# Optimization experiments

Measured on AMD Instinct MI355X. Metric: run time of the kernel, lower is better.

The kernel has to match this reference:

```python
import jax, jax.numpy as jnp
import numpy as np

K = 4        # maximum_fertility + 1
OOV_ID = 1
HIDDEN = 512


def setup_inputs() -> dict:
    key = jax.random.key(0)
    ks = jax.random.split(key, 8)
    B, S, D, E, H, V = 4, 128, 512, 256, HIDDEN, 32000
    return {
        "embedded_input": jax.random.normal(ks[0], (B, S, D), jnp.float32),
        "input_mask": jnp.ones((B, S), jnp.int32),
        "emb_table": jax.random.normal(ks[1], (V, E), jnp.float32) * 0.02,
        "W_ih": jax.random.normal(ks[2], (4 * H, D + E), jnp.float32) * 0.02,
        "b_ih": jax.random.normal(ks[3], (4 * H,), jnp.float32) * 0.02,
        "W_hh": jax.random.normal(ks[4], (4 * H, H), jnp.float32) * 0.02,
        "b_hh": jax.random.normal(ks[5], (4 * H,), jnp.float32) * 0.02,
        "W_out": jax.random.normal(ks[6], (V, H), jnp.float32) * 0.02,
        "b_out": jax.random.normal(ks[7], (V,), jnp.float32) * 0.02,
    }


def reference(embedded_input, input_mask, emb_table, W_ih, b_ih, W_hh, b_hh, W_out, b_out):
    B, S, D = embedded_input.shape
    V, E = emb_table.shape
    H = HIDDEN
    N = B * S
    x = embedded_input.reshape(N, D)                      # (N, D)
    h0 = jnp.zeros((N, H), embedded_input.dtype)
    c0 = jnp.zeros((N, H), embedded_input.dtype)
    # initial last_output: one-hot at OOV id (prob mass 1.0 on oov)
    last0 = jnp.zeros((N, V), embedded_input.dtype).at[:, OOV_ID].set(1.0)

    def step(carry, _):
        h, c, last = carry
        # embedding_bag soft mix over full vocab == weighted sum == matmul
        emb_last = last @ emb_table                        # (N, E)
        inp = jnp.concatenate([x, emb_last], axis=1)       # (N, D+E)
        gates = inp @ W_ih.T + b_ih + h @ W_hh.T + b_hh    # (N, 4H)
        i, f, g, o = jnp.split(gates, 4, axis=1)           # torch LSTMCell gate order
        i = jax.nn.sigmoid(i)
        f = jax.nn.sigmoid(f)
        g = jnp.tanh(g)
        o = jax.nn.sigmoid(o)
        c_new = f * c + i * g
        h_new = o * jnp.tanh(c_new)
        # dropout=0 / eval -> dropout mask is all ones (no-op)
        logits = h_new @ W_out.T + b_out                   # (N, V)
        logp = jax.nn.log_softmax(logits, axis=-1)
        return (h_new, c_new, jnp.exp(logp)), logp

    _, outs = jax.lax.scan(step, (h0, c0, last0), None, length=K)  # (K, N, V)
    return outs.transpose(1, 0, 2).reshape(B, S, K, V)
```

## Files before the change

### kernel.cpp

```cpp
#include <hip/hip_runtime.h>
#include <hip/hip_bf16.h>
#include <math.h>

#define N_ROWS 512
#define D_IN   512
#define E_EMB  256
#define H_DIM  512
#define G_DIM  2048
#define V_DIM  32000
#define IN_LD  1280
#define K_STEPS 4
#define OOV_ID 1
#define TBK 64
#define EMB_SPLIT 50
#define EMB_CHUNK 640
#define SEGSTRIDE 512

typedef __attribute__((ext_vector_type(4))) float f32x4;
typedef __attribute__((ext_vector_type(8))) short bf16x8;
typedef __attribute__((ext_vector_type(8))) _Float16 f16x8;

__device__ inline short f2b(float v) {
    __hip_bfloat16 h = __float2bfloat16(v);
    return *reinterpret_cast<short*>(&h);
}

__device__ inline void gload_lds(const short* g, short* l) {
    __builtin_amdgcn_global_load_lds(
        (const __attribute__((address_space(1))) void*)g,
        (__attribute__((address_space(3))) void*)l, 16, 0, 0);
}

template<int TBM, int TBN, int WR_, int WC_, int MODE>
__global__ __launch_bounds__(WR_ * WC_ * 64) void k_gemm(
    const short* __restrict__ A, int lda,
    const short* __restrict__ B, int ldb,
    const float* __restrict__ bias,
    float* __restrict__ C, size_t ldc, int Kc,
    float2* __restrict__ stats,
    float* __restrict__ cstate, short* __restrict__ hdst)
{
    constexpr int NW = WR_ * WC_;
    constexpr int WMT = TBM / WR_, WNT = TBN / WC_;
    constexpr int WM = WMT / 16, WN = WNT / 16;
    __shared__ short As[TBM * 64];
    __shared__ short Bs[TBN * 64];
    const int tid = threadIdx.x;
    const int lane = tid & 63, wid = tid >> 6;
    const int wr = wid % WR_, wc = wid / WR_;
    const int quad = lane >> 4, l16 = lane & 15;
    const int m0 = blockIdx.y * TBM, n0 = blockIdx.x * TBN;
    const int kbase = blockIdx.z * Kc;
    const int lrow = lane >> 3;
    const int lsw  = ((lane & 7) ^ lrow) * 8;

    f32x4 acc[WM][WN];
#pragma unroll
    for (int i = 0; i < WM; ++i)
#pragma unroll
        for (int j = 0; j < WN; ++j)
#pragma unroll
            for (int r = 0; r < 4; ++r) acc[i][j][r] = 0.0f;

    for (int kt = 0; kt < Kc; kt += TBK) {
        const int k0 = kbase + kt;
#pragma unroll
        for (int ch = wid; ch < TBM / 8; ch += NW)
            gload_lds(&A[(size_t)(m0 + ch * 8 + lrow) * lda + k0 + lsw], &As[ch * 512]);
#pragma unroll
        for (int ch = wid; ch < TBN / 8; ch += NW)
            gload_lds(&B[(size_t)(n0 + ch * 8 + lrow) * ldb + k0 + lsw], &Bs[ch * 512]);
        __syncthreads();
#pragma unroll
        for (int ks = 0; ks < 2; ++ks) {
            bf16x8 af[WM], bfv[WN];
#pragma unroll
            for (int i = 0; i < WM; ++i) {
                int rr = wr * WMT + i * 16 + l16;
                af[i] = *(const bf16x8*)&As[rr * 64 + (((ks * 4 + quad) ^ (l16 & 7)) * 8)];
            }
#pragma unroll
            for (int j = 0; j < WN; ++j) {
                int rr = wc * WNT + j * 16 + l16;
                bfv[j] = *(const bf16x8*)&Bs[rr * 64 + (((ks * 4 + quad) ^ (l16 & 7)) * 8)];
            }
#pragma unroll
            for (int i = 0; i < WM; ++i)
#pragma unroll
                for (int j = 0; j < WN; ++j)
                    acc[i][j] = __builtin_amdgcn_mfma_f32_16x16x32_bf16(af[i], bfv[j], acc[i][j], 0, 0, 0);
        }
        __syncthreads();
    }

    if constexpr (MODE == 3) {
        float* Cp = C + (size_t)blockIdx.z * N_ROWS * ldc;
#pragma unroll
        for (int i = 0; i < WM; ++i)
#pragma unroll
            for (int j = 0; j < WN; ++j) {
                const int n = n0 + wc * WNT + j * 16 + l16;
#pragma unroll
                for (int r = 0; r < 4; ++r) {
                    const int m = m0 + wr * WMT + i * 16 + quad * 4 + r;
                    Cp[(size_t)m * ldc + n] = acc[i][j][r];
                }
            }
    } else if constexpr (MODE == 2) {
        float bv[WN];
#pragma unroll
        for (int j = 0; j < WN; ++j) bv[j] = bias[n0 + j * 16 + l16];
        const int jj = (n0 >> 2) + l16;
#pragma unroll
        for (int i = 0; i < WM; ++i) {
#pragma unroll
            for (int r = 0; r < 4; ++r) {
                const int m = m0 + wr * WMT + i * 16 + quad * 4 + r;
                float gi = acc[i][0][r] + bv[0];
                float gf = acc[i][1][r] + bv[1];
                float gg = acc[i][2][r] + bv[2];
                float go = acc[i][3][r] + bv[3];
                float i_ = 1.0f / (1.0f + expf(-gi));
                float f_ = 1.0f / (1.0f + expf(-gf));
                float g_ = tanhf(gg);
                float o_ = 1.0f / (1.0f + expf(-go));
                const size_t ci = (size_t)m * H_DIM + jj;
                float cn = f_ * cstate[ci] + i_ * g_;
                cstate[ci] = cn;
                hdst[(size_t)m * IN_LD + (D_IN + E_EMB) + jj] = f2b(o_ * tanhf(cn));
            }
        }
    } else if constexpr (MODE == 4) {
        _Float16* Ch = (_Float16*)C;
        float bv[WN];
#pragma unroll
        for (int j = 0; j < WN; ++j) bv[j] = bias[n0 + wc * WNT + j * 16 + l16];
#pragma unroll
        for (int i = 0; i < WM; ++i) {
            float rm[4] = {-1e30f, -1e30f, -1e30f, -1e30f};
            float rs[4] = {0.f, 0.f, 0.f, 0.f};
#pragma unroll
            for (int j = 0; j < WN; ++j)
#pragma unroll
                for (int r = 0; r < 4; ++r)
                    rm[r] = fmaxf(rm[r], acc[i][j][r] + bv[j]);
#pragma unroll
            for (int j = 0; j < WN; ++j) {
                const int n = n0 + wc * WNT + j * 16 + l16;
#pragma unroll
                for (int r = 0; r < 4; ++r) {
                    const int m = m0 + wr * WMT + i * 16 + quad * 4 + r;
                    float z = acc[i][j][r] + bv[j];
                    rs[r] += __expf(z - rm[r]);
                    Ch[(size_t)m * ldc + n] = (_Float16)z;
                }
            }
#pragma unroll
            for (int mask = 1; mask < 16; mask <<= 1) {
#pragma unroll
                for (int r = 0; r < 4; ++r) {
                    float om = __shfl_xor(rm[r], mask);
                    float os = __shfl_xor(rs[r], mask);
                    float nm = fmaxf(rm[r], om);
                    rs[r] = rs[r] * __expf(rm[r] - nm) + os * __expf(om - nm);
                    rm[r] = nm;
                }
            }
            if (l16 == 0) {
                const int seg = (n0 + wc * WNT) >> 6;
#pragma unroll
                for (int r = 0; r < 4; ++r) {
                    const int m = m0 + wr * WMT + i * 16 + quad * 4 + r;
                    stats[(size_t)m * SEGSTRIDE + seg] = make_float2(rm[r], rs[r]);
                }
            }
        }
    } else {
        float bv[WN];
#pragma unroll
        for (int j = 0; j < WN; ++j) bv[j] = bias[n0 + wc * WNT + j * 16 + l16];
#pragma unroll
        for (int i = 0; i < WM; ++i)
#pragma unroll
            for (int j = 0; j < WN; ++j) {
                const int n = n0 + wc * WNT + j * 16 + l16;
#pragma unroll
                for (int r = 0; r < 4; ++r) {
                    const int m = m0 + wr * WMT + i * 16 + quad * 4 + r;
                    C[(size_t)m * ldc + n] = acc[i][j][r] + bv[j];
                }
            }
    }
}

__global__ __launch_bounds__(256) void k_prep(
    const float* __restrict__ x, const float* __restrict__ emb_table,
    const float* __restrict__ W_ih, const float* __restrict__ W_hh,
    const float* __restrict__ b_ih, const float* __restrict__ b_hh,
    const float* __restrict__ W_out,
    short* __restrict__ Abuf, short* __restrict__ Wg, float* __restrict__ bsum,
    short* __restrict__ Wout16, float* __restrict__ c)
{
    const int idx0 = blockIdx.x * 256 + threadIdx.x;
    const int gs = gridDim.x * 256;
    const float4* W4 = (const float4*)W_out;
    for (int i = idx0; i < V_DIM * H_DIM / 4; i += gs) {
        float4 v = W4[i];
        short4 o;
        o.x = f2b(v.x); o.y = f2b(v.y); o.z = f2b(v.z); o.w = f2b(v.w);
        ((short4*)Wout16)[i] = o;
    }
    for (int i = idx0; i < G_DIM * IN_LD; i += gs) {
        int rp = i / IN_LD, k = i - rp * IN_LD;
        int j = ((rp >> 6) << 4) | (rp & 15);
        int gate = (rp >> 4) & 3;
        int g = gate * H_DIM + j;
        float v = (k < D_IN + E_EMB) ? W_ih[(size_t)g * (D_IN + E_EMB) + k]
                                     : W_hh[(size_t)g * H_DIM + (k - (D_IN + E_EMB))];
        Wg[i] = f2b(v);
    }
    for (int i = idx0; i < G_DIM; i += gs) {
        int j = ((i >> 6) << 4) | (i & 15);
        int gate = (i >> 4) & 3;
        int g = gate * H_DIM + j;
        bsum[i] = b_ih[g] + b_hh[g];
    }
    for (int i = idx0; i < N_ROWS * IN_LD; i += gs) {
        int n = i / IN_LD, col = i - n * IN_LD;
        float v;
        if (col < D_IN)              v = x[(size_t)n * D_IN + col];
        else if (col < D_IN + E_EMB) v = emb_table[(size_t)OOV_ID * E_EMB + (col - D_IN)];
        else                         v = 0.0f;
        Abuf[i] = f2b(v);
    }
    for (int i = idx0; i < N_ROWS * H_DIM; i += gs) c[i] = 0.0f;
}

__global__ __launch_bounds__(256) void k_trans(const float* __restrict__ emb,
                                               short* __restrict__ embT)
{
    __shared__ float tile[64][65];
    const int v0 = blockIdx.x * 64, e0 = blockIdx.y * 64;
    const int tid = threadIdx.x;
#pragma unroll
    for (int i = 0; i < 16; ++i) {
        int idx = tid + i * 256;
        int vr = idx >> 6, ec = idx & 63;
        tile[vr][ec] = emb[(size_t)(v0 + vr) * E_EMB + e0 + ec];
    }
    __syncthreads();
#pragma unroll
    for (int i = 0; i < 16; ++i) {
        int idx = tid + i * 256;
        int er = idx >> 6, vc = idx & 63;
        embT[(size_t)(e0 + er) * V_DIM + v0 + vc] = f2b(tile[vc][er]);
    }
}

__global__ __launch_bounds__(256) void k_embred(const float* __restrict__ ep,
                                                short* __restrict__ Abuf)
{
    int idx = blockIdx.x * 256 + threadIdx.x;
    int n = idx >> 8, e = idx & 255;
    float s0 = 0.f, s1 = 0.f;
#pragma unroll
    for (int z = 0; z < EMB_SPLIT; z += 2) {
        s0 += ep[((size_t)z * N_ROWS + n) * E_EMB + e];
        s1 += ep[((size_t)(z + 1) * N_ROWS + n) * E_EMB + e];
    }
    Abuf[(size_t)n * IN_LD + D_IN + e] = f2b(s0 + s1);
}

__global__ __launch_bounds__(256) void k_lse(const float2* __restrict__ stats,
                                             float* __restrict__ lse)
{
    const int tid = threadIdx.x;
    const int lane = tid & 63, wid = tid >> 6;
    const int n = blockIdx.x * 4 + wid;

    float m = -1e30f, s = 0.0f;
    for (int sg = lane; sg < V_DIM / 64; sg += 64) {
        float2 p = stats[(size_t)n * SEGSTRIDE + sg];
        float nm = fmaxf(m, p.x);
        s = s * __expf(m - nm) + p.y * __expf(p.x - nm);
        m = nm;
    }
#pragma unroll
    for (int mask = 32; mask > 0; mask >>= 1) {
        float om = __shfl_xor(m, mask);
        float os = __shfl_xor(s, mask);
        float nm = fmaxf(m, om);
        s = s * __expf(m - nm) + os * __expf(om - nm);
        m = nm;
    }
    if (lane == 0) lse[n] = m + __logf(s);
}

__global__ __launch_bounds__(256) void k_finish(const _Float16* __restrict__ zbuf,
                                                float* __restrict__ out,
                                                short* __restrict__ last,
                                                const float* __restrict__ lse,
                                                int step, int feed)
{
    const int n = blockIdx.y;
    const float l = lse[n];
    const f16x8* zr = (const f16x8*)(zbuf + (size_t)n * V_DIM);
    float4* row4 = (float4*)(out + ((size_t)n * K_STEPS + step) * V_DIM);
    bf16x8* prow = (bf16x8*)(last + (size_t)n * V_DIM);
#pragma unroll
    for (int it = 0; it < 2; ++it) {
        const int slot = threadIdx.x + it * 256;
        if (slot < 500) {
            const int cidx = blockIdx.x * 500 + slot;
            f16x8 zv = zr[cidx];
            float lp[8];
#pragma unroll
            for (int k = 0; k < 8; ++k) lp[k] = (float)zv[k] - l;
            row4[cidx * 2]     = make_float4(lp[0], lp[1], lp[2], lp[3]);
            row4[cidx * 2 + 1] = make_float4(lp[4], lp[5], lp[6], lp[7]);
            if (feed) {
                bf16x8 p;
#pragma unroll
                for (int k = 0; k < 8; ++k) p[k] = f2b(__expf(lp[k]));
                prow[cidx] = p;
            }
        }
    }
}

extern "C" void kernel_launch(void* const* d_in, const int* in_sizes, int n_in,
                              void* d_out, int out_size, void* d_ws, size_t ws_size,
                              hipStream_t stream) {
    (void)in_sizes; (void)n_in; (void)out_size; (void)ws_size;
    const float* x       = (const float*)d_in[0];
    const float* emb_tab = (const float*)d_in[2];
    const float* W_ih    = (const float*)d_in[3];
    const float* b_ih    = (const float*)d_in[4];
    const float* W_hh    = (const float*)d_in[5];
    const float* b_hh    = (const float*)d_in[6];
    const float* W_out   = (const float*)d_in[7];
    const float* b_out   = (const float*)d_in[8];
    float* out = (float*)d_out;

    char* ws = (char*)d_ws;
    short* Abuf   = (short*)ws;  ws += (size_t)N_ROWS * IN_LD * sizeof(short);
    float* c      = (float*)ws;  ws += (size_t)N_ROWS * H_DIM * sizeof(float);
    short* last   = (short*)ws;  ws += (size_t)N_ROWS * V_DIM * sizeof(short);
    short* Wout16 = (short*)ws;  ws += (size_t)V_DIM * H_DIM * sizeof(short);
    short* Wg     = (short*)ws;  ws += (size_t)G_DIM * IN_LD * sizeof(short);
    float* bsum   = (float*)ws;  ws += (size_t)G_DIM * sizeof(float);
    short* embT   = (short*)ws;  ws += (size_t)E_EMB * V_DIM * sizeof(short);
    float2* stats = (float2*)ws; ws += (size_t)N_ROWS * SEGSTRIDE * sizeof(float2);
    float* lse    = (float*)ws;  ws += (size_t)N_ROWS * sizeof(float);
    ws = (char*)(((size_t)ws + 255) & ~(size_t)255);
    _Float16* zbuf = (_Float16*)ws;
    float* epart   = (float*)ws;
    ws += (size_t)N_ROWS * V_DIM * sizeof(_Float16);

    k_prep<<<2048, 256, 0, stream>>>(x, emb_tab, W_ih, W_hh, b_ih, b_hh, W_out,
                                     Abuf, Wg, bsum, Wout16, c);
    k_trans<<<dim3(V_DIM / 64, E_EMB / 64), 256, 0, stream>>>(emb_tab, embT);

    for (int t = 0; t < K_STEPS; ++t) {
        if (t > 0) {
            k_gemm<128, 256, 2, 4, 3><<<dim3(1, N_ROWS / 128, EMB_SPLIT), 512, 0, stream>>>(
                last, V_DIM, embT, V_DIM, nullptr, epart, E_EMB, EMB_CHUNK,
                nullptr, nullptr, nullptr);
            k_embred<<<N_ROWS * E_EMB / 256, 256, 0, stream>>>(epart, Abuf);
        }
        k_gemm<64, 64, 4, 1, 2><<<dim3(G_DIM / 64, N_ROWS / 64, 1), 256, 0, stream>>>(
            Abuf, IN_LD, Wg, IN_LD, bsum, nullptr, 0, IN_LD, nullptr, c, Abuf);
        k_gemm<256, 128, 4, 2, 4><<<dim3(V_DIM / 128, N_ROWS / 256, 1), 512, 0, stream>>>(
            Abuf + (D_IN + E_EMB), IN_LD, Wout16, H_DIM, b_out,
            (float*)zbuf, V_DIM, H_DIM, stats, nullptr, nullptr);
        const int feed = (t < K_STEPS - 1) ? 1 : 0;
        k_lse<<<N_ROWS / 4, 256, 0, stream>>>(stats, lse);
        k_finish<<<dim3(8, N_ROWS), 256, 0, stream>>>(zbuf, out, last, lse, t, feed);
    }
}
```

Measured before the change: 692.8 us.

## Hoist step-invariant x·W_ih projection out of the LSTM loop

The input projection x@W_ih[:, :D] plus both biases does not change across steps, so it is now computed once before the loop into a gates0 buffer. Each step's gate GEMM then starts its accumulators from gates0 and only multiplies over the embedding and hidden columns (K=768 instead of 1280). The embedding split-K factor is also doubled, with smaller chunks per split. This adds an extra fp32 N×4H buffer that is read each step and a larger partial-sum reduction.

```diff
diff --git a/kernel.cpp b/kernel.cpp
--- a/kernel.cpp
+++ b/kernel.cpp
@@ -9,11 +9,12 @@
 #define G_DIM  2048
 #define V_DIM  32000
 #define IN_LD  1280
+#define KG     768
 #define K_STEPS 4
 #define OOV_ID 1
 #define TBK 64
-#define EMB_SPLIT 50
-#define EMB_CHUNK 640
+#define EMB_SPLIT 100
+#define EMB_CHUNK 320
 #define SEGSTRIDE 512
 
 typedef __attribute__((ext_vector_type(4))) float f32x4;
@@ -31,7 +32,7 @@
         (__attribute__((address_space(3))) void*)l, 16, 0, 0);
 }
 
-template<int TBM, int TBN, int WR_, int WC_, int MODE>
+template<int TBM, int TBN, int WR_, int WC_, int MODE, int INITC>
 __global__ __launch_bounds__(WR_ * WC_ * 64) void k_gemm(
     const short* __restrict__ A, int lda,
     const short* __restrict__ B, int ldb,
@@ -55,12 +56,26 @@
     const int lsw  = ((lane & 7) ^ lrow) * 8;
 
     f32x4 acc[WM][WN];
-#pragma unroll
-    for (int i = 0; i < WM; ++i)
-#pragma unroll
-        for (int j = 0; j < WN; ++j)
-#pragma unroll
-            for (int r = 0; r < 4; ++r) acc[i][j][r] = 0.0f;
+    if constexpr (INITC) {
+#pragma unroll
+        for (int i = 0; i < WM; ++i)
+#pragma unroll
+            for (int j = 0; j < WN; ++j) {
+                const int n = n0 + wc * WNT + j * 16 + l16;
+#pragma unroll
+                for (int r = 0; r < 4; ++r) {
+                    const int m = m0 + wr * WMT + i * 16 + quad * 4 + r;
+                    acc[i][j][r] = C[(size_t)m * ldc + n];
+                }
+            }
+    } else {
+#pragma unroll
+        for (int i = 0; i < WM; ++i)
+#pragma unroll
+            for (int j = 0; j < WN; ++j)
+#pragma unroll
+                for (int r = 0; r < 4; ++r) acc[i][j][r] = 0.0f;
+    }
 
     for (int kt = 0; kt < Kc; kt += TBK) {
         const int k0 = kbase + kt;
@@ -109,7 +124,7 @@
     } else if constexpr (MODE == 2) {
         float bv[WN];
 #pragma unroll
-        for (int j = 0; j < WN; ++j) bv[j] = bias[n0 + j * 16 + l16];
+        for (int j = 0; j < WN; ++j) bv[j] = INITC ? 0.0f : bias[n0 + j * 16 + l16];
         const int jj = (n0 >> 2) + l16;
 #pragma unroll
         for (int i = 0; i < WM; ++i) {
@@ -198,8 +213,8 @@
     const float* __restrict__ W_ih, const float* __restrict__ W_hh,
     const float* __restrict__ b_ih, const float* __restrict__ b_hh,
     const float* __restrict__ W_out,
-    short* __restrict__ Abuf, short* __restrict__ Wg, float* __restrict__ bsum,
-    short* __restrict__ Wout16, float* __restrict__ c)
+    short* __restrict__ Abuf, short* __restrict__ Wg, short* __restrict__ Wx16,
+    float* __restrict__ bsum, short* __restrict__ Wout16, float* __restrict__ c)
 {
     const int idx0 = blockIdx.x * 256 + threadIdx.x;
     const int gs = gridDim.x * 256;
@@ -210,14 +225,21 @@
         o.x = f2b(v.x); o.y = f2b(v.y); o.z = f2b(v.z); o.w = f2b(v.w);
         ((short4*)Wout16)[i] = o;
     }
-    for (int i = idx0; i < G_DIM * IN_LD; i += gs) {
-        int rp = i / IN_LD, k = i - rp * IN_LD;
+    for (int i = idx0; i < G_DIM * KG; i += gs) {
+        int rp = i / KG, k = i - rp * KG;
         int j = ((rp >> 6) << 4) | (rp & 15);
         int gate = (rp >> 4) & 3;
         int g = gate * H_DIM + j;
-        float v = (k < D_IN + E_EMB) ? W_ih[(size_t)g * (D_IN + E_EMB) + k]
-                                     : W_hh[(size_t)g * H_DIM + (k - (D_IN + E_EMB))];
+        float v = (k < E_EMB) ? W_ih[(size_t)g * (D_IN + E_EMB) + D_IN + k]
+                              : W_hh[(size_t)g * H_DIM + (k - E_EMB)];
         Wg[i] = f2b(v);
+    }
+    for (int i = idx0; i < G_DIM * D_IN; i += gs) {
+        int rp = i / D_IN, k = i - rp * D_IN;
+        int j = ((rp >> 6) << 4) | (rp & 15);
+        int gate = (rp >> 4) & 3;
+        int g = gate * H_DIM + j;
+        Wx16[i] = f2b(W_ih[(size_t)g * (D_IN + E_EMB) + k]);
     }
     for (int i = idx0; i < G_DIM; i += gs) {
         int j = ((i >> 6) << 4) | (i & 15);
@@ -263,7 +285,7 @@
     int idx = blockIdx.x * 256 + threadIdx.x;
     int n = idx >> 8, e = idx & 255;
     float s0 = 0.f, s1 = 0.f;
-#pragma unroll
+#pragma unroll 2
     for (int z = 0; z < EMB_SPLIT; z += 2) {
         s0 += ep[((size_t)z * N_ROWS + n) * E_EMB + e];
         s1 += ep[((size_t)(z + 1) * N_ROWS + n) * E_EMB + e];
@@ -347,30 +369,34 @@
     float* c      = (float*)ws;  ws += (size_t)N_ROWS * H_DIM * sizeof(float);
     short* last   = (short*)ws;  ws += (size_t)N_ROWS * V_DIM * sizeof(short);
     short* Wout16 = (short*)ws;  ws += (size_t)V_DIM * H_DIM * sizeof(short);
-    short* Wg     = (short*)ws;  ws += (size_t)G_DIM * IN_LD * sizeof(short);
+    short* Wg     = (short*)ws;  ws += (size_t)G_DIM * KG * sizeof(short);
+    short* Wx16   = (short*)ws;  ws += (size_t)G_DIM * D_IN * sizeof(short);
     float* bsum   = (float*)ws;  ws += (size_t)G_DIM * sizeof(float);
+    float* gates0 = (float*)ws;  ws += (size_t)N_ROWS * G_DIM * sizeof(float);
     short* embT   = (short*)ws;  ws += (size_t)E_EMB * V_DIM * sizeof(short);
     float2* stats = (float2*)ws; ws += (size_t)N_ROWS * SEGSTRIDE * sizeof(float2);
     float* lse    = (float*)ws;  ws += (size_t)N_ROWS * sizeof(float);
     ws = (char*)(((size_t)ws + 255) & ~(size_t)255);
     _Float16* zbuf = (_Float16*)ws;
     float* epart   = (float*)ws;
-    ws += (size_t)N_ROWS * V_DIM * sizeof(_Float16);
+    ws += (size_t)EMB_SPLIT * N_ROWS * E_EMB * sizeof(float);
 
     k_prep<<<2048, 256, 0, stream>>>(x, emb_tab, W_ih, W_hh, b_ih, b_hh, W_out,
-                                     Abuf, Wg, bsum, Wout16, c);
+                                     Abuf, Wg, Wx16, bsum, Wout16, c);
     k_trans<<<dim3(V_DIM / 64, E_EMB / 64), 256, 0, stream>>>(emb_tab, embT);
+    k_gemm<64, 64, 4, 1, 0, 0><<<dim3(G_DIM / 64, N_ROWS / 64, 1), 256, 0, stream>>>(
+        Abuf, IN_LD, Wx16, D_IN, bsum, gates0, G_DIM, D_IN, nullptr, nullptr, nullptr);
 
     for (int t = 0; t < K_STEPS; ++t) {
         if (t > 0) {
-            k_gemm<128, 256, 2, 4, 3><<<dim3(1, N_ROWS / 128, EMB_SPLIT), 512, 0, stream>>>(
+            k_gemm<128, 256, 2, 4, 3, 0><<<dim3(1, N_ROWS / 128, EMB_SPLIT), 512, 0, stream>>>(
                 last, V_DIM, embT, V_DIM, nullptr, epart, E_EMB, EMB_CHUNK,
                 nullptr, nullptr, nullptr);
             k_embred<<<N_ROWS * E_EMB / 256, 256, 0, stream>>>(epart, Abuf);
         }
-        k_gemm<64, 64, 4, 1, 2><<<dim3(G_DIM / 64, N_ROWS / 64, 1), 256, 0, stream>>>(
-            Abuf, IN_LD, Wg, IN_LD, bsum, nullptr, 0, IN_LD, nullptr, c, Abuf);
-        k_gemm<256, 128, 4, 2, 4><<<dim3(V_DIM / 128, N_ROWS / 256, 1), 512, 0, stream>>>(
+        k_gemm<64, 64, 4, 1, 2, 1><<<dim3(G_DIM / 64, N_ROWS / 64, 1), 256, 0, stream>>>(
+            Abuf + D_IN, IN_LD, Wg, KG, nullptr, gates0, G_DIM, KG, nullptr, c, Abuf);
+        k_gemm<256, 128, 4, 2, 4, 0><<<dim3(V_DIM / 128, N_ROWS / 256, 1), 512, 0, stream>>>(
             Abuf + (D_IN + E_EMB), IN_LD, Wout16, H_DIM, b_out,
             (float*)zbuf, V_DIM, H_DIM, stats, nullptr, nullptr);
         const int feed = (t < K_STEPS - 1) ? 1 : 0;
```

Result: no change. 702.1 us (+1.3%).

## Fuse log-softmax finish and prob conversion into embedding-bag GEMM A-load

Applied to the files above, without the earlier changes.

The embedding-bag GEMM now reads the fp16 logits directly, subtracts the log-sum-exp, writes the log-prob output rows, and converts exp(logp) to bf16 in LDS as its A operand. This removes the separate finish kernel and the bf16 probability buffer for the first three steps. A standalone finish runs only after the last step. It replaces the async global-to-LDS load with register loads plus exp work inside the GEMM, which may slow the GEMM main loop. The epart buffer is no longer aliased with zbuf, and the reduction loop unroll is reduced.

```diff
diff --git a/kernel.cpp b/kernel.cpp
--- a/kernel.cpp
+++ b/kernel.cpp
@@ -38,7 +38,8 @@
     const float* __restrict__ bias,
     float* __restrict__ C, size_t ldc, int Kc,
     float2* __restrict__ stats,
-    float* __restrict__ cstate, short* __restrict__ hdst)
+    float* __restrict__ cstate, short* __restrict__ hdst,
+    float* __restrict__ outdst, size_t ldout, const float* __restrict__ lsep)
 {
     constexpr int NW = WR_ * WC_;
     constexpr int WMT = TBM / WR_, WNT = TBN / WC_;
@@ -64,12 +65,36 @@
 
     for (int kt = 0; kt < Kc; kt += TBK) {
         const int k0 = kbase + kt;
-#pragma unroll
-        for (int ch = wid; ch < TBM / 8; ch += NW)
-            gload_lds(&A[(size_t)(m0 + ch * 8 + lrow) * lda + k0 + lsw], &As[ch * 512]);
-#pragma unroll
-        for (int ch = wid; ch < TBN / 8; ch += NW)
-            gload_lds(&B[(size_t)(n0 + ch * 8 + lrow) * ldb + k0 + lsw], &Bs[ch * 512]);
+        if constexpr (MODE == 5) {
+#pragma unroll
+            for (int ch = wid; ch < TBN / 8; ch += NW)
+                gload_lds(&B[(size_t)(n0 + ch * 8 + lrow) * ldb + k0 + lsw], &Bs[ch * 512]);
+            const _Float16* Z = (const _Float16*)A;
+#pragma unroll
+            for (int ch = wid; ch < TBM / 8; ch += NW) {
+                const int row = m0 + ch * 8 + lrow;
+                const int col = k0 + lsw;
+                f16x8 zv = *(const f16x8*)&Z[(size_t)row * lda + col];
+                const float l = lsep[row];
+                float lp[8];
+#pragma unroll
+                for (int q = 0; q < 8; ++q) lp[q] = (float)zv[q] - l;
+                float4* od = (float4*)&outdst[(size_t)row * ldout + col];
+                od[0] = make_float4(lp[0], lp[1], lp[2], lp[3]);
+                od[1] = make_float4(lp[4], lp[5], lp[6], lp[7]);
+                bf16x8 p;
+#pragma unroll
+                for (int q = 0; q < 8; ++q) p[q] = f2b(__expf(lp[q]));
+                *(bf16x8*)&As[ch * 512 + lane * 8] = p;
+            }
+        } else {
+#pragma unroll
+            for (int ch = wid; ch < TBM / 8; ch += NW)
+                gload_lds(&A[(size_t)(m0 + ch * 8 + lrow) * lda + k0 + lsw], &As[ch * 512]);
+#pragma unroll
+            for (int ch = wid; ch < TBN / 8; ch += NW)
+                gload_lds(&B[(size_t)(n0 + ch * 8 + lrow) * ldb + k0 + lsw], &Bs[ch * 512]);
+        }
         __syncthreads();
 #pragma unroll
         for (int ks = 0; ks < 2; ++ks) {
@@ -93,7 +118,7 @@
         __syncthreads();
     }
 
-    if constexpr (MODE == 3) {
+    if constexpr (MODE == 3 || MODE == 5) {
         float* Cp = C + (size_t)blockIdx.z * N_ROWS * ldc;
 #pragma unroll
         for (int i = 0; i < WM; ++i)
@@ -263,7 +288,7 @@
     int idx = blockIdx.x * 256 + threadIdx.x;
     int n = idx >> 8, e = idx & 255;
     float s0 = 0.f, s1 = 0.f;
-#pragma unroll
+#pragma unroll 2
     for (int z = 0; z < EMB_SPLIT; z += 2) {
         s0 += ep[((size_t)z * N_ROWS + n) * E_EMB + e];
         s1 += ep[((size_t)(z + 1) * N_ROWS + n) * E_EMB + e];
@@ -298,15 +323,13 @@
 
 __global__ __launch_bounds__(256) void k_finish(const _Float16* __restrict__ zbuf,
                                                 float* __restrict__ out,
-                                                short* __restrict__ last,
                                                 const float* __restrict__ lse,
-                                                int step, int feed)
+                                                int step)
 {
     const int n = blockIdx.y;
     const float l = lse[n];
     const f16x8* zr = (const f16x8*)(zbuf + (size_t)n * V_DIM);
     float4* row4 = (float4*)(out + ((size_t)n * K_STEPS + step) * V_DIM);
-    bf16x8* prow = (bf16x8*)(last + (size_t)n * V_DIM);
 #pragma unroll
     for (int it = 0; it < 2; ++it) {
         const int slot = threadIdx.x + it * 256;
@@ -318,12 +341,6 @@
             for (int k = 0; k < 8; ++k) lp[k] = (float)zv[k] - l;
             row4[cidx * 2]     = make_float4(lp[0], lp[1], lp[2], lp[3]);
             row4[cidx * 2 + 1] = make_float4(lp[4], lp[5], lp[6], lp[7]);
-            if (feed) {
-                bf16x8 p;
-#pragma unroll
-                for (int k = 0; k < 8; ++k) p[k] = f2b(__expf(lp[k]));
-                prow[cidx] = p;
-            }
         }
     }
 }
@@ -345,7 +362,6 @@
     char* ws = (char*)d_ws;
     short* Abuf   = (short*)ws;  ws += (size_t)N_ROWS * IN_LD * sizeof(short);
     float* c      = (float*)ws;  ws += (size_t)N_ROWS * H_DIM * sizeof(float);
-    short* last   = (short*)ws;  ws += (size_t)N_ROWS * V_DIM * sizeof(short);
     short* Wout16 = (short*)ws;  ws += (size_t)V_DIM * H_DIM * sizeof(short);
     short* Wg     = (short*)ws;  ws += (size_t)G_DIM * IN_LD * sizeof(short);
     float* bsum   = (float*)ws;  ws += (size_t)G_DIM * sizeof(float);
@@ -353,9 +369,8 @@
     float2* stats = (float2*)ws; ws += (size_t)N_ROWS * SEGSTRIDE * sizeof(float2);
     float* lse    = (float*)ws;  ws += (size_t)N_ROWS * sizeof(float);
     ws = (char*)(((size_t)ws + 255) & ~(size_t)255);
-    _Float16* zbuf = (_Float16*)ws;
-    float* epart   = (float*)ws;
-    ws += (size_t)N_ROWS * V_DIM * sizeof(_Float16);
+    _Float16* zbuf = (_Float16*)ws; ws += (size_t)N_ROWS * V_DIM * sizeof(_Float16);
+    float* epart   = (float*)ws;    ws += (size_t)EMB_SPLIT * N_ROWS * E_EMB * sizeof(float);
 
     k_prep<<<2048, 256, 0, stream>>>(x, emb_tab, W_ih, W_hh, b_ih, b_hh, W_out,
                                      Abuf, Wg, bsum, Wout16, c);
@@ -363,18 +378,21 @@
 
     for (int t = 0; t < K_STEPS; ++t) {
         if (t > 0) {
-            k_gemm<128, 256, 2, 4, 3><<<dim3(1, N_ROWS / 128, EMB_SPLIT), 512, 0, stream>>>(
-                last, V_DIM, embT, V_DIM, nullptr, epart, E_EMB, EMB_CHUNK,
-                nullptr, nullptr, nullptr);
+            k_lse<<<N_ROWS / 4, 256, 0, stream>>>(stats, lse);
+            k_gemm<128, 256, 2, 4, 5><<<dim3(1, N_ROWS / 128, EMB_SPLIT), 512, 0, stream>>>(
+                (const short*)zbuf, V_DIM, embT, V_DIM, nullptr, epart, E_EMB, EMB_CHUNK,
+                nullptr, nullptr, nullptr,
+                out + (size_t)(t - 1) * V_DIM, (size_t)K_STEPS * V_DIM, lse);
             k_embred<<<N_ROWS * E_EMB / 256, 256, 0, stream>>>(epart, Abuf);
         }
         k_gemm<64, 64, 4, 1, 2><<<dim3(G_DIM / 64, N_ROWS / 64, 1), 256, 0, stream>>>(
-            Abuf, IN_LD, Wg, IN_LD, bsum, nullptr, 0, IN_LD, nullptr, c, Abuf);
+            Abuf, IN_LD, Wg, IN_LD, bsum, nullptr, 0, IN_LD, nullptr, c, Abuf,
+            nullptr, 0, nullptr);
         k_gemm<256, 128, 4, 2, 4><<<dim3(V_DIM / 128, N_ROWS / 256, 1), 512, 0, stream>>>(
             Abuf + (D_IN + E_EMB), IN_LD, Wout16, H_DIM, b_out,
-            (float*)zbuf, V_DIM, H_DIM, stats, nullptr, nullptr);
-        const int feed = (t < K_STEPS - 1) ? 1 : 0;
-        k_lse<<<N_ROWS / 4, 256, 0, stream>>>(stats, lse);
-        k_finish<<<dim3(8, N_ROWS), 256, 0, stream>>>(zbuf, out, last, lse, t, feed);
-    }
-}
+            (float*)zbuf, V_DIM, H_DIM, stats, nullptr, nullptr,
+            nullptr, 0, nullptr);
+    }
+    k_lse<<<N_ROWS / 4, 256, 0, stream>>>(stats, lse);
+    k_finish<<<dim3(8, N_ROWS), 256, 0, stream>>>(zbuf, out, lse, K_STEPS - 1);
+}
```

Result: faster. 670.3 us (-3.3%).
